# Performance work log

Measured on AMD Instinct MI355X. Metric: run time of the kernel, lower is better.

## Reference

```python
import jax, jax.numpy as jnp
import numpy as np

V, H, B = 64, 128, 16384  # num_visible, num_hidden = alpha*V, batch of spin configs
ISCALE = 0.001


def setup_inputs() -> dict:
    key = jax.random.key(0)
    k1, k2, k3, k4 = jax.random.split(key, 4)
    x = jax.random.normal(k1, (B, V), dtype=jnp.float32)
    weight_1 = jax.random.normal(k2, (V, H), dtype=jnp.float32) * ISCALE
    weight_2 = jax.random.normal(k3, (H, V, V), dtype=jnp.float32) * (ISCALE / 10.0)
    hidden_bias = jax.random.normal(k4, (H,), dtype=jnp.float32) * ISCALE
    return {"x": x, "weight_1": weight_1, "weight_2": weight_2, "hidden_bias": hidden_bias}


def reference(x, weight_1, weight_2, hidden_bias):
    b, v = x.shape
    h = weight_2.shape[0]
    # order-1 term: (B,V) @ (V,H) -> (B,H)
    w1 = x @ weight_1
    # order-2 term: outer product of spins per sample, contracted with weight_2.
    # vis_ij: (B,V,V) flattened to (B,V*V); weight_2 flattened to (H,V*V) -> GEMM.
    vis_ij = jnp.einsum('mi,mj->mij', x, x).reshape(b, v * v)
    w2 = (vis_ij @ weight_2.reshape(h, v * v).T) * 0.5
    act = jnp.cos(hidden_bias + w1 + w2)  # (B,H)
    psi = jnp.prod(act, axis=-1)          # (B,)
    return psi
```

## Files before the change

### kernel.cpp

```cpp
#include <hip/hip_runtime.h>
#include <hip/hip_bf16.h>
#include <cstdint>

#define NV 64
#define NH 128
#define NB 16384
#define NCHUNK 37

typedef __bf16 bf16x8_t __attribute__((ext_vector_type(8)));
typedef float f32x16_t __attribute__((ext_vector_type(16)));
typedef float f32x2_t __attribute__((ext_vector_type(2)));
typedef uint32_t u32x4_t __attribute__((ext_vector_type(4)));
typedef uint32_t u32x2_t __attribute__((ext_vector_type(2)));

__device__ __forceinline__ uint32_t bf16_rne(float f) {
  uint32_t u = __float_as_uint(f);
  return (u + 0x7fffu + ((u >> 16) & 1u)) >> 16;
}

__global__ void cvt_kernel(const float* __restrict__ w1f,
                           const float* __restrict__ w2f,
                           uint8_t* __restrict__ frag) {
  __shared__ float W[4096];
  __shared__ float w1c[64];
  const int tid = threadIdx.x;
  const int h = blockIdx.x;
  {
    const float* src = w2f + (size_t)h * 4096;
#pragma unroll
    for (int u = 0; u < 4; ++u)
      *(float4*)(&W[u * 1024 + tid * 4]) =
          *(const float4*)(src + u * 1024 + tid * 4);
  }
  if (tid < 64) w1c[tid] = w1f[tid * 128 + h];
  __syncthreads();
  const int fh2 = h >> 5, hl = h & 31;
  for (int idx = tid; idx < 296; idx += 256) {
    int c = idx >> 3, kk = (idx >> 1) & 3, lh = idx & 1;
    int a = kk * 2 + lh;
    float v[8];
    if (c < 8) {
      int ib = (c * 8 + a) * 64 + c * 8;
#pragma unroll
      for (int t = 0; t < 8; ++t) v[t] = 0.5f * W[ib + t];
    } else if (c < 36) {
      int o = c - 8, I = 0;
      while (o >= 7 - I) { o -= 7 - I; ++I; }
      int J = I + 1 + o;
      int i = I * 8 + a;
#pragma unroll
      for (int t = 0; t < 8; ++t) {
        int j = J * 8 + t;
        v[t] = 0.5f * (W[i * 64 + j] + W[j * 64 + i]);
      }
    } else {
      int sb = kk * 16 + lh * 8;
#pragma unroll
      for (int t = 0; t < 8; ++t) v[t] = w1c[sb + t];
    }
    uint4 o4;
    o4.x = (bf16_rne(v[1]) << 16) | bf16_rne(v[0]);
    o4.y = (bf16_rne(v[3]) << 16) | bf16_rne(v[2]);
    o4.z = (bf16_rne(v[5]) << 16) | bf16_rne(v[4]);
    o4.w = (bf16_rne(v[7]) << 16) | bf16_rne(v[6]);
    *(uint4*)(frag + ((size_t)((c * 4 + kk) * 4 + fh2) << 10) +
              ((lh * 32 + hl) << 4)) = o4;
  }
}

__device__ __forceinline__ uint32_t pack2(f32x2_t pr) {
  u32x2_t u = __builtin_bit_cast(u32x2_t, pr);
  return __builtin_amdgcn_perm(u[1], u[0], 0x07060302);
}

template <int C0, int C1>
__device__ __forceinline__ void kloop(const uint8_t* pw, const f32x2_t* xb,
                                      int lh, f32x16_t& acc, bf16x8_t* bn) {
  constexpr int CI[36] = {0,1,2,3,4,5,6,7, 0,0,0,0,0,0,0, 1,1,1,1,1,1,
                          2,2,2,2,2, 3,3,3,3, 4,4,4, 5,5, 6};
  constexpr int CJ[36] = {0,1,2,3,4,5,6,7, 1,2,3,4,5,6,7, 2,3,4,5,6,7,
                          3,4,5,6,7, 4,5,6,7, 5,6,7, 6,7, 7};
#pragma unroll
  for (int c = C0; c < C1; ++c) {
    bf16x8_t bc[4];
#pragma unroll
    for (int kk = 0; kk < 4; ++kk) bc[kk] = bn[kk];
    const uint8_t* pn = pw + (size_t)(c + 1) * 16384;
#pragma unroll
    for (int kk = 0; kk < 4; ++kk)
      bn[kk] = *(const bf16x8_t*)(pn + kk * 4096);
    const int I = CI[c], J = CJ[c];
#pragma unroll
    for (int kk = 0; kk < 4; ++kk) {
      f32x2_t sp = xb[I * 4 + kk];
      float s = lh ? sp.y : sp.x;
      f32x2_t s2 = {s, s};
      u32x4_t adv;
#pragma unroll
      for (int tt = 0; tt < 4; ++tt)
        adv[tt] = pack2(s2 * xb[J * 4 + tt]);
      acc = __builtin_amdgcn_mfma_f32_32x32x16_bf16(
          __builtin_bit_cast(bf16x8_t, adv), bc[kk], acc, 0, 0, 0);
    }
  }
}

__launch_bounds__(512, 4)
__global__ void rbm_main(const float* __restrict__ xg,
                         const uint8_t* __restrict__ frag,
                         float* __restrict__ P) {
  const int tid = threadIdx.x;
  const int wv = tid >> 6;
  const int wm = wv & 1;
  const int hq = wv >> 1;
  const int lane = tid & 63;
  const int l31 = lane & 31;
  const int lh = lane >> 5;
  const int mblk = blockIdx.x * 64;
  const int ks = blockIdx.y;

  f32x2_t xb[32];
  {
    const float* p = xg + (size_t)(mblk + wm * 32 + l31) * NV;
#pragma unroll
    for (int g = 0; g < 16; ++g) {
      float4 v = *(const float4*)(p + g * 4);
      xb[g * 2] = f32x2_t{v.x, v.y};
      xb[g * 2 + 1] = f32x2_t{v.z, v.w};
    }
  }

  const uint8_t* pw = frag + hq * 1024 + (size_t)lane * 16;
  f32x16_t acc = (f32x16_t)0.0f;
  bf16x8_t bn[4];
  {
    const uint8_t* p0 = pw + (size_t)(ks ? 18 : 0) * 16384;
#pragma unroll
    for (int kk = 0; kk < 4; ++kk)
      bn[kk] = *(const bf16x8_t*)(p0 + kk * 4096);
  }

  if (ks == 0) {
    kloop<0, 18>(pw, xb, lh, acc, bn);
  } else {
    kloop<18, 36>(pw, xb, lh, acc, bn);
#pragma unroll
    for (int kk = 0; kk < 4; ++kk) {
      u32x4_t adv;
#pragma unroll
      for (int tt = 0; tt < 4; ++tt) {
        f32x2_t v = lh ? xb[kk * 8 + 4 + tt] : xb[kk * 8 + tt];
        adv[tt] = pack2(v);
      }
      acc = __builtin_amdgcn_mfma_f32_32x32x16_bf16(
          __builtin_bit_cast(bf16x8_t, adv), bn[kk], acc, 0, 0, 0);
    }
  }

  float* pp = P + ((size_t)(ks * NB + mblk + wm * 32)) * NH + hq * 32 + l31;
#pragma unroll
  for (int r = 0; r < 16; ++r) {
    int mloc = (r & 3) + 8 * (r >> 2) + 4 * lh;
    pp[(size_t)mloc * NH] = acc[r];
  }
}

__global__ void reduce_kernel(const float* __restrict__ P,
                              const float* __restrict__ biasg,
                              float* __restrict__ outg) {
  const int tid = threadIdx.x;
  const int wv = tid >> 6;
  const int lane = tid & 63;
  const int m0 = blockIdx.x * 16 + wv * 4;
  const float b0 = biasg[lane], b1 = biasg[64 + lane];
  const float INV2PI = 0.15915494309189535f;
#pragma unroll
  for (int u = 0; u < 4; ++u) {
    const int m = m0 + u;
    const float* p0 = P + (size_t)m * NH;
    const float* p1 = P + (size_t)(NB + m) * NH;
    float a0 = p0[lane] + p1[lane] + b0;
    float a1 = p0[64 + lane] + p1[64 + lane] + b1;
    float pr = __builtin_amdgcn_cosf(a0 * INV2PI) *
               __builtin_amdgcn_cosf(a1 * INV2PI);
#pragma unroll
    for (int ofs = 1; ofs < 64; ofs <<= 1)
      pr *= __shfl_xor(pr, ofs, 64);
    if (lane == 0) outg[m] = pr;
  }
}

extern "C" void kernel_launch(void* const* d_in, const int* in_sizes, int n_in,
                              void* d_out, int out_size, void* d_ws, size_t ws_size,
                              hipStream_t stream) {
  const float* x   = (const float*)d_in[0];
  const float* w1f = (const float*)d_in[1];
  const float* w2f = (const float*)d_in[2];
  const float* hb  = (const float*)d_in[3];
  float* out = (float*)d_out;
  uint8_t* frag = (uint8_t*)d_ws;
  float* P = (float*)((uint8_t*)d_ws + (1 << 20));
  (void)in_sizes; (void)n_in; (void)out_size; (void)ws_size;

  cvt_kernel<<<128, 256, 0, stream>>>(w1f, w2f, frag);
  rbm_main<<<dim3(NB / 64, 2), 512, 0, stream>>>(x, frag, P);
  reduce_kernel<<<NB / 16, 256, 0, stream>>>(P, hb, out);
}
```

Measured before the change: 96.20 us.

## Fuse cosine-product epilogue into GEMM kernel and drop split-K partials

```diff
diff --git a/kernel.cpp b/kernel.cpp
--- a/kernel.cpp
+++ b/kernel.cpp
@@ -73,22 +73,58 @@
   return __builtin_amdgcn_perm(u[1], u[0], 0x07060302);
 }
 
-template <int C0, int C1>
-__device__ __forceinline__ void kloop(const uint8_t* pw, const f32x2_t* xb,
-                                      int lh, f32x16_t& acc, bf16x8_t* bn) {
+__launch_bounds__(512, 2)
+__global__ void rbm_main(const float* __restrict__ xg,
+                         const float* __restrict__ biasg,
+                         const uint8_t* __restrict__ frag,
+                         float* __restrict__ outg) {
+  __shared__ float part[4][64];
   constexpr int CI[36] = {0,1,2,3,4,5,6,7, 0,0,0,0,0,0,0, 1,1,1,1,1,1,
                           2,2,2,2,2, 3,3,3,3, 4,4,4, 5,5, 6};
   constexpr int CJ[36] = {0,1,2,3,4,5,6,7, 1,2,3,4,5,6,7, 2,3,4,5,6,7,
                           3,4,5,6,7, 4,5,6,7, 5,6,7, 6,7, 7};
+
+  const int tid = threadIdx.x;
+  const int wv = tid >> 6;
+  const int wm = wv & 1;
+  const int hq = wv >> 1;
+  const int lane = tid & 63;
+  const int l31 = lane & 31;
+  const int lh = lane >> 5;
+  const int mblk = blockIdx.x * 64;
+
+  f32x2_t xb[32];
+  {
+    const float* p = xg + (size_t)(mblk + wm * 32 + l31) * NV;
 #pragma unroll
-  for (int c = C0; c < C1; ++c) {
+    for (int g = 0; g < 16; ++g) {
+      float4 v = *(const float4*)(p + g * 4);
+      xb[g * 2] = f32x2_t{v.x, v.y};
+      xb[g * 2 + 1] = f32x2_t{v.z, v.w};
+    }
+  }
+
+  const uint8_t* pw = frag + hq * 1024 + (size_t)lane * 16;
+  f32x16_t acc = (f32x16_t)0.0f;
+
+  bf16x8_t bn[2][4];
+#pragma unroll
+  for (int d = 0; d < 2; ++d)
+#pragma unroll
+    for (int kk = 0; kk < 4; ++kk)
+      bn[d][kk] = *(const bf16x8_t*)(pw + (size_t)d * 16384 + kk * 4096);
+
+#pragma unroll
+  for (int c = 0; c < 36; ++c) {
     bf16x8_t bc[4];
 #pragma unroll
-    for (int kk = 0; kk < 4; ++kk) bc[kk] = bn[kk];
-    const uint8_t* pn = pw + (size_t)(c + 1) * 16384;
+    for (int kk = 0; kk < 4; ++kk) bc[kk] = bn[c & 1][kk];
+    if (c + 2 <= 36) {
+      const uint8_t* pn = pw + (size_t)(c + 2) * 16384;
 #pragma unroll
-    for (int kk = 0; kk < 4; ++kk)
-      bn[kk] = *(const bf16x8_t*)(pn + kk * 4096);
+      for (int kk = 0; kk < 4; ++kk)
+        bn[c & 1][kk] = *(const bf16x8_t*)(pn + kk * 4096);
+    }
     const int I = CI[c], J = CJ[c];
 #pragma unroll
     for (int kk = 0; kk < 4; ++kk) {
@@ -103,90 +139,42 @@
           __builtin_bit_cast(bf16x8_t, adv), bc[kk], acc, 0, 0, 0);
     }
   }
-}
+#pragma unroll
+  for (int kk = 0; kk < 4; ++kk) {
+    u32x4_t adv;
+#pragma unroll
+    for (int tt = 0; tt < 4; ++tt) {
+      f32x2_t v = lh ? xb[kk * 8 + 4 + tt] : xb[kk * 8 + tt];
+      adv[tt] = pack2(v);
+    }
+    acc = __builtin_amdgcn_mfma_f32_32x32x16_bf16(
+        __builtin_bit_cast(bf16x8_t, adv), bn[0][kk], acc, 0, 0, 0);
+  }
 
-__launch_bounds__(512, 4)
-__global__ void rbm_main(const float* __restrict__ xg,
-                         const uint8_t* __restrict__ frag,
-                         float* __restrict__ P) {
-  const int tid = threadIdx.x;
-  const int wv = tid >> 6;
-  const int wm = wv & 1;
-  const int hq = wv >> 1;
-  const int lane = tid & 63;
-  const int l31 = lane & 31;
-  const int lh = lane >> 5;
-  const int mblk = blockIdx.x * 64;
-  const int ks = blockIdx.y;
+  const float INV2PI = 0.15915494309189535f;
+  const float bs = biasg[hq * 32 + l31];
+  float pr[16];
+#pragma unroll
+  for (int r = 0; r < 16; ++r)
+    pr[r] = __builtin_amdgcn_cosf((acc[r] + bs) * INV2PI);
 
-  f32x2_t xb[32];
-  {
-    const float* p = xg + (size_t)(mblk + wm * 32 + l31) * NV;
 #pragma unroll
-    for (int g = 0; g < 16; ++g) {
-      float4 v = *(const float4*)(p + g * 4);
-      xb[g * 2] = f32x2_t{v.x, v.y};
-      xb[g * 2 + 1] = f32x2_t{v.z, v.w};
+  for (int ofs = 1; ofs < 32; ofs <<= 1)
+#pragma unroll
+    for (int r = 0; r < 16; ++r)
+      pr[r] *= __shfl_xor(pr[r], ofs, 32);
+
+  if (l31 == 0) {
+#pragma unroll
+    for (int r = 0; r < 16; ++r) {
+      int mloc = (r & 3) + 8 * (r >> 2) + 4 * lh;
+      part[hq][wm * 32 + mloc] = pr[r];
     }
   }
-
-  const uint8_t* pw = frag + hq * 1024 + (size_t)lane * 16;
-  f32x16_t acc = (f32x16_t)0.0f;
-  bf16x8_t bn[4];
-  {
-    const uint8_t* p0 = pw + (size_t)(ks ? 18 : 0) * 16384;
-#pragma unroll
-    for (int kk = 0; kk < 4; ++kk)
-      bn[kk] = *(const bf16x8_t*)(p0 + kk * 4096);
-  }
-
-  if (ks == 0) {
-    kloop<0, 18>(pw, xb, lh, acc, bn);
-  } else {
-    kloop<18, 36>(pw, xb, lh, acc, bn);
-#pragma unroll
-    for (int kk = 0; kk < 4; ++kk) {
-      u32x4_t adv;
-#pragma unroll
-      for (int tt = 0; tt < 4; ++tt) {
-        f32x2_t v = lh ? xb[kk * 8 + 4 + tt] : xb[kk * 8 + tt];
-        adv[tt] = pack2(v);
-      }
-      acc = __builtin_amdgcn_mfma_f32_32x32x16_bf16(
-          __builtin_bit_cast(bf16x8_t, adv), bn[kk], acc, 0, 0, 0);
-    }
-  }
-
-  float* pp = P + ((size_t)(ks * NB + mblk + wm * 32)) * NH + hq * 32 + l31;
-#pragma unroll
-  for (int r = 0; r < 16; ++r) {
-    int mloc = (r & 3) + 8 * (r >> 2) + 4 * lh;
-    pp[(size_t)mloc * NH] = acc[r];
-  }
-}
-
-__global__ void reduce_kernel(const float* __restrict__ P,
-                              const float* __restrict__ biasg,
-                              float* __restrict__ outg) {
-  const int tid = threadIdx.x;
-  const int wv = tid >> 6;
-  const int lane = tid & 63;
-  const int m0 = blockIdx.x * 16 + wv * 4;
-  const float b0 = biasg[lane], b1 = biasg[64 + lane];
-  const float INV2PI = 0.15915494309189535f;
-#pragma unroll
-  for (int u = 0; u < 4; ++u) {
-    const int m = m0 + u;
-    const float* p0 = P + (size_t)m * NH;
-    const float* p1 = P + (size_t)(NB + m) * NH;
-    float a0 = p0[lane] + p1[lane] + b0;
-    float a1 = p0[64 + lane] + p1[64 + lane] + b1;
-    float pr = __builtin_amdgcn_cosf(a0 * INV2PI) *
-               __builtin_amdgcn_cosf(a1 * INV2PI);
-#pragma unroll
-    for (int ofs = 1; ofs < 64; ofs <<= 1)
-      pr *= __shfl_xor(pr, ofs, 64);
-    if (lane == 0) outg[m] = pr;
+  __syncthreads();
+  if (tid < 64) {
+    float f = part[0][tid] * part[1][tid] * part[2][tid] * part[3][tid];
+    outg[mblk + tid] = f;
   }
 }
 
@@ -199,10 +187,8 @@
   const float* hb  = (const float*)d_in[3];
   float* out = (float*)d_out;
   uint8_t* frag = (uint8_t*)d_ws;
-  float* P = (float*)((uint8_t*)d_ws + (1 << 20));
   (void)in_sizes; (void)n_in; (void)out_size; (void)ws_size;
 
   cvt_kernel<<<128, 256, 0, stream>>>(w1f, w2f, frag);
-  rbm_main<<<dim3(NB / 64, 2), 512, 0, stream>>>(x, frag, P);
-  reduce_kernel<<<NB / 16, 256, 0, stream>>>(P, hb, out);
+  rbm_main<<<NB / 64, 512, 0, stream>>>(x, hb, frag, out);
 }
```

New measurement: 100.8 us. 1.05x slower.

## Reuse each B fragment across two M tiles, split K three ways, pack x as bf16

Applied to the files above, without the earlier changes.

```diff
diff --git a/kernel.cpp b/kernel.cpp
--- a/kernel.cpp
+++ b/kernel.cpp
@@ -6,6 +6,7 @@
 #define NH 128
 #define NB 16384
 #define NCHUNK 37
+#define PSLICE (NB * NH)
 
 typedef __bf16 bf16x8_t __attribute__((ext_vector_type(8)));
 typedef float f32x16_t __attribute__((ext_vector_type(16)));
@@ -74,8 +75,9 @@
 }
 
 template <int C0, int C1>
-__device__ __forceinline__ void kloop(const uint8_t* pw, const f32x2_t* xb,
-                                      int lh, f32x16_t& acc, bf16x8_t* bn) {
+__device__ __forceinline__ void kloop(const uint8_t* pw,
+                                      const uint32_t xpk[2][32], int lh,
+                                      f32x16_t acc[2]) {
   constexpr int CI[36] = {0,1,2,3,4,5,6,7, 0,0,0,0,0,0,0, 1,1,1,1,1,1,
                           2,2,2,2,2, 3,3,3,3, 4,4,4, 5,5, 6};
   constexpr int CJ[36] = {0,1,2,3,4,5,6,7, 1,2,3,4,5,6,7, 2,3,4,5,6,7,
@@ -84,85 +86,88 @@
   for (int c = C0; c < C1; ++c) {
     bf16x8_t bc[4];
 #pragma unroll
-    for (int kk = 0; kk < 4; ++kk) bc[kk] = bn[kk];
-    const uint8_t* pn = pw + (size_t)(c + 1) * 16384;
-#pragma unroll
     for (int kk = 0; kk < 4; ++kk)
-      bn[kk] = *(const bf16x8_t*)(pn + kk * 4096);
+      bc[kk] = *(const bf16x8_t*)(pw + (size_t)c * 16384 + kk * 4096);
     const int I = CI[c], J = CJ[c];
 #pragma unroll
     for (int kk = 0; kk < 4; ++kk) {
-      f32x2_t sp = xb[I * 4 + kk];
-      float s = lh ? sp.y : sp.x;
-      f32x2_t s2 = {s, s};
-      u32x4_t adv;
-#pragma unroll
-      for (int tt = 0; tt < 4; ++tt)
-        adv[tt] = pack2(s2 * xb[J * 4 + tt]);
-      acc = __builtin_amdgcn_mfma_f32_32x32x16_bf16(
-          __builtin_bit_cast(bf16x8_t, adv), bc[kk], acc, 0, 0, 0);
-    }
-  }
-}
-
-__launch_bounds__(512, 4)
+#pragma unroll
+      for (int im = 0; im < 2; ++im) {
+        uint32_t su = xpk[im][I * 4 + kk];
+        uint32_t sb = lh ? (su & 0xffff0000u) : (su << 16);
+        float s = __uint_as_float(sb);
+        f32x2_t s2 = {s, s};
+        u32x4_t adv;
+#pragma unroll
+        for (int tt = 0; tt < 4; ++tt) {
+          uint32_t xu = xpk[im][J * 4 + tt];
+          f32x2_t xv = {__uint_as_float(xu << 16),
+                        __uint_as_float(xu & 0xffff0000u)};
+          adv[tt] = pack2(s2 * xv);
+        }
+        acc[im] = __builtin_amdgcn_mfma_f32_32x32x16_bf16(
+            __builtin_bit_cast(bf16x8_t, adv), bc[kk], acc[im], 0, 0, 0);
+      }
+    }
+  }
+}
+
+__launch_bounds__(256, 3)
 __global__ void rbm_main(const float* __restrict__ xg,
                          const uint8_t* __restrict__ frag,
                          float* __restrict__ P) {
   const int tid = threadIdx.x;
-  const int wv = tid >> 6;
-  const int wm = wv & 1;
-  const int hq = wv >> 1;
+  const int hq = tid >> 6;
   const int lane = tid & 63;
   const int l31 = lane & 31;
   const int lh = lane >> 5;
   const int mblk = blockIdx.x * 64;
   const int ks = blockIdx.y;
 
-  f32x2_t xb[32];
-  {
-    const float* p = xg + (size_t)(mblk + wm * 32 + l31) * NV;
+  uint32_t xpk[2][32];
+#pragma unroll
+  for (int im = 0; im < 2; ++im) {
+    const float* p = xg + (size_t)(mblk + im * 32 + l31) * NV;
 #pragma unroll
     for (int g = 0; g < 16; ++g) {
       float4 v = *(const float4*)(p + g * 4);
-      xb[g * 2] = f32x2_t{v.x, v.y};
-      xb[g * 2 + 1] = f32x2_t{v.z, v.w};
+      xpk[im][g * 2]     = (bf16_rne(v.y) << 16) | bf16_rne(v.x);
+      xpk[im][g * 2 + 1] = (bf16_rne(v.w) << 16) | bf16_rne(v.z);
     }
   }
 
   const uint8_t* pw = frag + hq * 1024 + (size_t)lane * 16;
-  f32x16_t acc = (f32x16_t)0.0f;
-  bf16x8_t bn[4];
-  {
-    const uint8_t* p0 = pw + (size_t)(ks ? 18 : 0) * 16384;
-#pragma unroll
-    for (int kk = 0; kk < 4; ++kk)
-      bn[kk] = *(const bf16x8_t*)(p0 + kk * 4096);
-  }
+  f32x16_t acc[2] = {(f32x16_t)0.0f, (f32x16_t)0.0f};
 
   if (ks == 0) {
-    kloop<0, 18>(pw, xb, lh, acc, bn);
+    kloop<0, 12>(pw, xpk, lh, acc);
+  } else if (ks == 1) {
+    kloop<12, 24>(pw, xpk, lh, acc);
   } else {
-    kloop<18, 36>(pw, xb, lh, acc, bn);
+    kloop<24, 36>(pw, xpk, lh, acc);
 #pragma unroll
     for (int kk = 0; kk < 4; ++kk) {
-      u32x4_t adv;
-#pragma unroll
-      for (int tt = 0; tt < 4; ++tt) {
-        f32x2_t v = lh ? xb[kk * 8 + 4 + tt] : xb[kk * 8 + tt];
-        adv[tt] = pack2(v);
+      bf16x8_t bt = *(const bf16x8_t*)(pw + (size_t)36 * 16384 + kk * 4096);
+#pragma unroll
+      for (int im = 0; im < 2; ++im) {
+        u32x4_t adv;
+#pragma unroll
+        for (int tt = 0; tt < 4; ++tt)
+          adv[tt] = xpk[im][kk * 8 + lh * 4 + tt];
+        acc[im] = __builtin_amdgcn_mfma_f32_32x32x16_bf16(
+            __builtin_bit_cast(bf16x8_t, adv), bt, acc[im], 0, 0, 0);
       }
-      acc = __builtin_amdgcn_mfma_f32_32x32x16_bf16(
-          __builtin_bit_cast(bf16x8_t, adv), bn[kk], acc, 0, 0, 0);
-    }
-  }
-
-  float* pp = P + ((size_t)(ks * NB + mblk + wm * 32)) * NH + hq * 32 + l31;
-#pragma unroll
-  for (int r = 0; r < 16; ++r) {
-    int mloc = (r & 3) + 8 * (r >> 2) + 4 * lh;
-    pp[(size_t)mloc * NH] = acc[r];
-  }
+    }
+  }
+
+  float* pp = P + (size_t)ks * PSLICE + (size_t)mblk * NH + hq * 32 + l31;
+#pragma unroll
+  for (int im = 0; im < 2; ++im)
+#pragma unroll
+    for (int r = 0; r < 16; ++r) {
+      int mloc = im * 32 + (r & 3) + 8 * (r >> 2) + 4 * lh;
+      pp[(size_t)mloc * NH] = acc[im][r];
+    }
 }
 
 __global__ void reduce_kernel(const float* __restrict__ P,
@@ -171,18 +176,20 @@
   const int tid = threadIdx.x;
   const int wv = tid >> 6;
   const int lane = tid & 63;
-  const int m0 = blockIdx.x * 16 + wv * 4;
-  const float b0 = biasg[lane], b1 = biasg[64 + lane];
+  const int m0 = blockIdx.x * 32 + wv * 8;
+  const float2 b2 = *(const float2*)(biasg + 2 * lane);
   const float INV2PI = 0.15915494309189535f;
 #pragma unroll
-  for (int u = 0; u < 4; ++u) {
+  for (int u = 0; u < 8; ++u) {
     const int m = m0 + u;
-    const float* p0 = P + (size_t)m * NH;
-    const float* p1 = P + (size_t)(NB + m) * NH;
-    float a0 = p0[lane] + p1[lane] + b0;
-    float a1 = p0[64 + lane] + p1[64 + lane] + b1;
-    float pr = __builtin_amdgcn_cosf(a0 * INV2PI) *
-               __builtin_amdgcn_cosf(a1 * INV2PI);
+    const float* pm = P + (size_t)m * NH + 2 * lane;
+    float2 a0 = *(const float2*)(pm);
+    float2 a1 = *(const float2*)(pm + PSLICE);
+    float2 a2 = *(const float2*)(pm + 2 * (size_t)PSLICE);
+    float ax = a0.x + a1.x + a2.x + b2.x;
+    float ay = a0.y + a1.y + a2.y + b2.y;
+    float pr = __builtin_amdgcn_cosf(ax * INV2PI) *
+               __builtin_amdgcn_cosf(ay * INV2PI);
 #pragma unroll
     for (int ofs = 1; ofs < 64; ofs <<= 1)
       pr *= __shfl_xor(pr, ofs, 64);
@@ -203,6 +210,6 @@
   (void)in_sizes; (void)n_in; (void)out_size; (void)ws_size;
 
   cvt_kernel<<<128, 256, 0, stream>>>(w1f, w2f, frag);
-  rbm_main<<<dim3(NB / 64, 2), 512, 0, stream>>>(x, frag, P);
-  reduce_kernel<<<NB / 16, 256, 0, stream>>>(P, hb, out);
-}
+  rbm_main<<<dim3(NB / 64, 3), 256, 0, stream>>>(x, frag, P);
+  reduce_kernel<<<NB / 32, 256, 0, stream>>>(P, hb, out);
+}
```

After: 138.0 us. 1.43x slower.
